# Kernel tuning notes

Measured on AMD Instinct MI355X. Metric: run time of the kernel, lower is better.

## Reference

```python
import jax, jax.numpy as jnp
import numpy as np

HEADS = 16
HEAD_DIM = 64
HIDDEN = HEADS * HEAD_DIM          # 1024
EXP = 4
QKVFF = HIDDEN * (3 + EXP)         # 7168
VFF = HIDDEN * (1 + EXP)           # 5120
B, L = 2, 2048
LN_EPS = 1e-5


def setup_inputs() -> dict:
    key = jax.random.key(0)
    k1, k2, k3 = jax.random.split(key, 3)
    x = jax.random.normal(k1, (B, L, HIDDEN), dtype=jnp.float32)
    W_in = jax.random.normal(k2, (HIDDEN, QKVFF), dtype=jnp.float32) * (HIDDEN ** -0.5)
    W_out = jax.random.normal(k3, (VFF, HIDDEN), dtype=jnp.float32) * (VFF ** -0.5)
    ln_w = jnp.ones((HIDDEN,), dtype=jnp.float32)
    ln_b = jnp.zeros((HIDDEN,), dtype=jnp.float32)
    return {"x": x, "ln_w": ln_w, "ln_b": ln_b, "W_in": W_in, "W_out": W_out}


def _rotary_tables(l, dtype):
    inv_freq = 1.0 / (10000.0 ** (jnp.arange(0, HEAD_DIM, 2, dtype=jnp.float32) / HEAD_DIM))
    t = jnp.arange(l, dtype=jnp.float32)
    freqs = t[:, None] * inv_freq[None, :]            # [l, d/2]
    emb = jnp.concatenate([freqs, freqs], axis=-1)     # [l, d]
    return jnp.cos(emb).astype(dtype), jnp.sin(emb).astype(dtype)


def _rotate_half(x):
    x1, x2 = jnp.split(x, 2, axis=-1)
    return jnp.concatenate([-x2, x1], axis=-1)


def reference(x, ln_w, ln_b, W_in, W_out):
    b, l, d = x.shape
    # shared LayerNorm
    mu = jnp.mean(x, axis=-1, keepdims=True)
    var = jnp.var(x, axis=-1, keepdims=True)
    xn = (x - mu) * jax.lax.rsqrt(var + LN_EPS) * ln_w + ln_b
    # fused in-projection
    h = xn @ W_in                                      # [b, l, qkvff]
    q, k, v, ff = jnp.split(h, [HIDDEN, 2 * HIDDEN, 3 * HIDDEN], axis=-1)
    q = q.reshape(b, l, HEADS, HEAD_DIM)
    k = k.reshape(b, l, HEADS, HEAD_DIM)
    v = v.reshape(b, l, HEADS, HEAD_DIM)
    # inline RoPE on q, k
    cos, sin = _rotary_tables(l, x.dtype)              # [l, d]
    cos = cos[None, :, None, :]
    sin = sin[None, :, None, :]
    q = q * cos + _rotate_half(q) * sin
    k = k * cos + _rotate_half(k) * sin
    # causal attention with explicit mask bias (as in the original)
    a = jnp.einsum('bihd,bjhd->bhij', q, k) * (HEAD_DIM ** -0.5)
    causal = jnp.tril(jnp.ones((l, l), dtype=a.dtype))
    a = a + (-1e10) * (1.0 - causal)
    a = jax.nn.softmax(a, axis=-1)
    o = jnp.einsum('bhij,bjhd->bihd', a, v).reshape(b, l, HIDDEN)
    # parallel FF branch
    ff = jax.nn.gelu(ff, approximate=False)
    return jnp.concatenate([o, ff], axis=-1) @ W_out
```

## Files before the change

### kernel.cpp

```cpp
#include <hip/hip_runtime.h>
#include <math.h>

#define HEADS 16
#define HEAD_DIM 64
#define HIDDEN 1024
#define NQKVFF 7168
#define VFF 5120
#define SEQ 2048
#define MROWS 4096

typedef unsigned short u16;
typedef __attribute__((ext_vector_type(8))) short bf16x8;
typedef __attribute__((ext_vector_type(4))) float f32x4;
typedef __attribute__((address_space(1))) void gas_void;
typedef __attribute__((address_space(3))) void las_void;

__device__ inline u16 f2bf(float f) {
    union { float f; unsigned u; } v; v.f = f;
    unsigned r = v.u + 0x7FFFu + ((v.u >> 16) & 1u);
    return (u16)(r >> 16);
}
__device__ inline float bf2f(u16 h) {
    union { unsigned u; float f; } v; v.u = ((unsigned)h) << 16;
    return v.f;
}

__global__ __launch_bounds__(256) void ln_kernel(const float* __restrict__ x,
        const float* __restrict__ w, const float* __restrict__ b,
        u16* __restrict__ xn) {
    int row = blockIdx.x;
    int tid = threadIdx.x;
    const float* xr = x + (size_t)row * HIDDEN;
    float4 v = ((const float4*)xr)[tid];
    float s = v.x + v.y + v.z + v.w;
    float sq = v.x * v.x + v.y * v.y + v.z * v.z + v.w * v.w;
    for (int off = 32; off > 0; off >>= 1) {
        s += __shfl_down(s, off, 64);
        sq += __shfl_down(sq, off, 64);
    }
    __shared__ float ls[4], lsq[4];
    int wid = tid >> 6, lane = tid & 63;
    if (lane == 0) { ls[wid] = s; lsq[wid] = sq; }
    __syncthreads();
    float ts = ls[0] + ls[1] + ls[2] + ls[3];
    float tsq = lsq[0] + lsq[1] + lsq[2] + lsq[3];
    float mu = ts * (1.0f / HIDDEN);
    float var = tsq * (1.0f / HIDDEN) - mu * mu;
    float rstd = rsqrtf(var + 1e-5f);
    float4 wv = ((const float4*)w)[tid];
    float4 bv = ((const float4*)b)[tid];
    ushort4 o;
    o.x = f2bf((v.x - mu) * rstd * wv.x + bv.x);
    o.y = f2bf((v.y - mu) * rstd * wv.y + bv.y);
    o.z = f2bf((v.z - mu) * rstd * wv.z + bv.z);
    o.w = f2bf((v.w - mu) * rstd * wv.w + bv.w);
    ((ushort4*)(xn + (size_t)row * HIDDEN))[tid] = o;
}

__global__ __launch_bounds__(256) void transpose_f2b(const float* __restrict__ in,
        u16* __restrict__ out, int R, int C) {
    __shared__ u16 tile[32][33];
    int c0 = blockIdx.x * 32, r0 = blockIdx.y * 32;
    int tx = threadIdx.x & 31, ty = threadIdx.x >> 5;
#pragma unroll
    for (int k = 0; k < 4; k++)
        tile[ty + k * 8][tx] = f2bf(in[(size_t)(r0 + ty + k * 8) * C + c0 + tx]);
    __syncthreads();
#pragma unroll
    for (int k = 0; k < 4; k++)
        out[(size_t)(c0 + ty + k * 8) * R + r0 + tx] = tile[tx][ty + k * 8];
}

__global__ __launch_bounds__(256) void transpose_v(const u16* __restrict__ h3,
        u16* __restrict__ out) {
    __shared__ u16 tile[32][33];
    int bh = blockIdx.x, it = blockIdx.y, dt = blockIdx.z;
    int bb = bh >> 4, hh = bh & 15;
    u16* dst = out + (size_t)bh * HEAD_DIM * SEQ;
    int tx = threadIdx.x & 31, ty = threadIdx.x >> 5;
    int i0 = it * 32, d0 = dt * 32;
#pragma unroll
    for (int k = 0; k < 4; k++)
        tile[ty + k * 8][tx] = h3[(size_t)(bb * 2048 + i0 + ty + k * 8) * 3072 + 2048 + hh * 64 + d0 + tx];
    __syncthreads();
#pragma unroll
    for (int k = 0; k < 4; k++) {
        int d = d0 + ty + k * 8;
        int i = i0 + tx;
        dst[(size_t)(i >> 5) * 2048 + (d >> 4) * 512 +
            ((((i & 31) >> 3) * 16) + (d & 15)) * 8 + (i & 7)] = tile[tx][ty + k * 8];
    }
}

__global__ __launch_bounds__(256) void rope_kernel(const u16* __restrict__ h3,
        u16* __restrict__ qk) {
    int idx = blockIdx.x * 256 + threadIdx.x;
    int j = idx & 31;
    int i = (idx >> 5) & 2047;
    int rest = idx >> 16;
    int t = rest >> 5, bh = rest & 31;
    int bb = bh >> 4, hh = bh & 15;
    const u16* src = h3 + ((size_t)(bb * 2048 + i)) * 3072 + t * 1024 + hh * 64;
    float x1 = bf2f(src[j]), x2 = bf2f(src[j + 32]);
    float f = expf(j * -0.28782313662425572f);
    float ang = i * f;
    float s, c;
    sincosf(ang, &s, &c);
    float scale = (t == 0) ? 0.18033688011112043f : 1.0f;
    u16* base = qk + (size_t)rest * (SEQ * HEAD_DIM);
    int off = (i >> 4) * 1024 + ((j >> 3) * 16 + (i & 15)) * 8 + (j & 7);
    base[off]       = f2bf((x1 * c - x2 * s) * scale);
    base[off + 512] = f2bf((x2 * c + x1 * s) * scale);
}

__device__ inline void gemm_core_128(const u16* __restrict__ A, int lda,
                                     const u16* __restrict__ BT, int ldb,
                                     int Klen, int bm, int bn, f32x4 acc[4][4],
                                     u16* ldsA, u16* ldsB) {
    const int tid = threadIdx.x;
    const int wid = tid >> 6;
    const int lane = tid & 63;
    const int quad = lane >> 4;
    const int cc = lane & 15;
    const int wm = (wid >> 1) * 64;
    const int wn = (wid & 1) * 64;
#pragma unroll
    for (int i = 0; i < 4; i++)
#pragma unroll
        for (int j = 0; j < 4; j++)
#pragma unroll
            for (int r = 0; r < 4; r++) acc[i][j][r] = 0.0f;

    const int row = tid >> 2;
    const int gch = ((tid & 3) ^ ((row >> 1) & 3)) * 8;
    const int slot = (quad ^ ((cc >> 1) & 3)) * 8;
    for (int k0 = 0; k0 < Klen; k0 += 32) {
        __syncthreads();
#pragma unroll
        for (int I = 0; I < 2; I++) {
            int r128 = I * 64 + row;
            const u16* ga = A + (size_t)(bm + r128) * lda + k0 + gch;
            u16* la = ldsA + ((size_t)(I * 256 + (tid & 192))) * 8;
            __builtin_amdgcn_global_load_lds((gas_void*)ga, (las_void*)la, 16, 0, 0);
            const u16* gb = BT + (size_t)(bn + r128) * ldb + k0 + gch;
            u16* lb = ldsB + ((size_t)(I * 256 + (tid & 192))) * 8;
            __builtin_amdgcn_global_load_lds((gas_void*)gb, (las_void*)lb, 16, 0, 0);
        }
        __syncthreads();
        bf16x8 af[4], bfr[4];
#pragma unroll
        for (int t = 0; t < 4; t++) {
            af[t]  = *(const bf16x8*)(ldsA + (wm + t * 16 + cc) * 32 + slot);
            bfr[t] = *(const bf16x8*)(ldsB + (wn + t * 16 + cc) * 32 + slot);
        }
#pragma unroll
        for (int i = 0; i < 4; i++)
#pragma unroll
            for (int j = 0; j < 4; j++)
                acc[i][j] = __builtin_amdgcn_mfma_f32_16x16x32_bf16(af[i], bfr[j], acc[i][j], 0, 0, 0);
    }
}

__device__ inline float gelu_f(float v) {
    float u = v * (v * v * 0.044715f + 1.0f) * 0.7978845608028654f;
    u = fminf(u, 15.0f);
    float e = exp2f(u * 2.8853900817779268f);
    return v * (e / (e + 1.0f));
}

__global__ __launch_bounds__(256) void gemm1(const u16* __restrict__ xn,
        const u16* __restrict__ WinT, u16* __restrict__ h3, u16* __restrict__ a2) {
    __shared__ u16 ldsA[128 * 32];
    __shared__ u16 ldsB[128 * 32];
    int bm = blockIdx.x * 128, bn = blockIdx.y * 128;
    f32x4 acc[4][4];
    gemm_core_128(xn, HIDDEN, WinT, HIDDEN, HIDDEN, bm, bn, acc, ldsA, ldsB);
    const int tid = threadIdx.x, wid = tid >> 6, lane = tid & 63;
    const int quad = lane >> 4, cc = lane & 15;
    const int wm = (wid >> 1) * 64, wn = (wid & 1) * 64;
    const bool isff = (bn >= 3072);
#pragma unroll
    for (int i = 0; i < 4; i++)
#pragma unroll
        for (int j = 0; j < 4; j++)
#pragma unroll
            for (int r = 0; r < 4; r++) {
                int m = bm + wm + i * 16 + quad * 4 + r;
                int n = bn + wn + j * 16 + cc;
                float v = acc[i][j][r];
                if (isff) {
                    a2[(size_t)m * VFF + (n - 2048)] = f2bf(gelu_f(v));
                } else {
                    h3[(size_t)m * 3072 + n] = f2bf(v);
                }
            }
}

__global__ __launch_bounds__(256) void gemm2(const u16* __restrict__ a2,
        const u16* __restrict__ WoutT, float* __restrict__ p0, float* __restrict__ p1) {
    __shared__ u16 ldsA[128 * 32];
    __shared__ u16 ldsB[128 * 32];
    int bm = blockIdx.x * 128, bn = blockIdx.y * 128;
    int split = blockIdx.z;
    float* dst = split ? p1 : p0;
    f32x4 acc[4][4];
    gemm_core_128(a2 + split * 2560, VFF, WoutT + split * 2560, VFF, 2560,
                  bm, bn, acc, ldsA, ldsB);
    const int tid = threadIdx.x, wid = tid >> 6, lane = tid & 63;
    const int quad = lane >> 4, cc = lane & 15;
    const int wm = (wid >> 1) * 64, wn = (wid & 1) * 64;
#pragma unroll
    for (int i = 0; i < 4; i++)
#pragma unroll
        for (int j = 0; j < 4; j++)
#pragma unroll
            for (int r = 0; r < 4; r++) {
                int m = bm + wm + i * 16 + quad * 4 + r;
                int n = bn + wn + j * 16 + cc;
                dst[(size_t)m * HIDDEN + n] = acc[i][j][r];
            }
}

__global__ __launch_bounds__(256) void reduce2(const float* __restrict__ p0,
        const float* __restrict__ p1, float* __restrict__ out) {
    int i = blockIdx.x * 256 + threadIdx.x;
    float4 a = ((const float4*)p0)[i];
    float4 b = ((const float4*)p1)[i];
    a.x += b.x; a.y += b.y; a.z += b.z; a.w += b.w;
    ((float4*)out)[i] = a;
}

__global__ __launch_bounds__(256) void attn_kernel(const u16* __restrict__ qk,
        const u16* __restrict__ vt, u16* __restrict__ a2) {
    const int id  = blockIdx.x;
    const int bh  = (id & 7) * 4 + ((id >> 3) & 3);
    const int bx  = id >> 5;
    const int tid = threadIdx.x;
    const int wid = tid >> 6;
    const int lane = tid & 63;
    const int quad = lane >> 4;
    const int cc = lane & 15;
    const int slot = wid >> 1;
    const int parity = wid & 1;
    const int tile = slot ? (127 - bx) : bx;
    const int q0 = tile * 16;

    const u16* Qp = qk + (size_t)bh * (SEQ * HEAD_DIM);
    const u16* Kp = qk + (size_t)(32 + bh) * (SEQ * HEAD_DIM);
    const u16* VP = vt + (size_t)bh * (HEAD_DIM * SEQ);

    __shared__ u16 Pbuf[4][16 * 72];
    __shared__ float obuf[2][64 * 17];
    __shared__ float lbuf[2][16];
    u16* P = Pbuf[wid];

    const int bb = bh >> 4, hh = bh & 15;
    const int qcol = q0 + cc;

    bf16x8 qa0 = *(const bf16x8*)(Qp + (q0 >> 4) * 1024 + lane * 8);
    bf16x8 qa1 = *(const bf16x8*)(Qp + (q0 >> 4) * 1024 + 512 + lane * 8);

    float ps = 0.0f;
    f32x4 ot[4];
#pragma unroll
    for (int mt = 0; mt < 4; mt++)
#pragma unroll
        for (int r = 0; r < 4; r++) ot[mt][r] = 0.0f;

    for (int kb = parity * 64; kb < q0 + 16; kb += 128) {
        const bool diag = (kb + 64 > q0);
        f32x4 s[4];
        __builtin_amdgcn_s_setprio(1);
#pragma unroll
        for (int c = 0; c < 4; c++) {
            s[c][0] = -32.0f; s[c][1] = -32.0f; s[c][2] = -32.0f; s[c][3] = -32.0f;
            const u16* kblob = Kp + ((kb >> 4) + c) * 1024 + lane * 8;
            bf16x8 ka0 = *(const bf16x8*)(kblob);
            bf16x8 ka1 = *(const bf16x8*)(kblob + 512);
            s[c] = __builtin_amdgcn_mfma_f32_16x16x32_bf16(ka0, qa0, s[c], 0, 0, 0);
            s[c] = __builtin_amdgcn_mfma_f32_16x16x32_bf16(ka1, qa1, s[c], 0, 0, 0);
        }
        __builtin_amdgcn_s_setprio(0);
        bf16x8 vf[2][4];
#pragma unroll
        for (int kc = 0; kc < 2; kc++)
#pragma unroll
            for (int mt = 0; mt < 4; mt++)
                vf[kc][mt] = *(const bf16x8*)(VP + ((kb >> 5) + kc) * 2048 + mt * 512 + lane * 8);
        if (diag) {
#pragma unroll
            for (int c = 0; c < 4; c++)
#pragma unroll
                for (int r = 0; r < 4; r++) {
                    int key = kb + c * 16 + quad * 4 + r;
                    s[c][r] = (key <= qcol) ? s[c][r] : -10000.0f;
                }
        }
#pragma unroll
        for (int c = 0; c < 4; c++) {
            float p0v = exp2f(s[c][0]); ps += p0v;
            float p1v = exp2f(s[c][1]); ps += p1v;
            float p2v = exp2f(s[c][2]); ps += p2v;
            float p3v = exp2f(s[c][3]); ps += p3v;
            unsigned r0, r1;
            asm("v_cvt_pk_bf16_f32 %0, %1, %2" : "=v"(r0) : "v"(p0v), "v"(p1v));
            asm("v_cvt_pk_bf16_f32 %0, %1, %2" : "=v"(r1) : "v"(p2v), "v"(p3v));
            uint2 pk; pk.x = r0; pk.y = r1;
            *(uint2*)(P + cc * 72 + c * 16 + quad * 4) = pk;
        }
        asm volatile("s_waitcnt lgkmcnt(0)" ::: "memory");
        __builtin_amdgcn_s_setprio(1);
#pragma unroll
        for (int kc = 0; kc < 2; kc++) {
            bf16x8 pb = *(const bf16x8*)(P + cc * 72 + kc * 32 + quad * 8);
#pragma unroll
            for (int mt = 0; mt < 4; mt++)
                ot[mt] = __builtin_amdgcn_mfma_f32_16x16x32_bf16(vf[kc][mt], pb, ot[mt], 0, 0, 0);
        }
        __builtin_amdgcn_s_setprio(0);
    }

    ps += __shfl_xor(ps, 16, 64);
    ps += __shfl_xor(ps, 32, 64);

    if (parity == 1) {
        if (quad == 0) lbuf[slot][cc] = ps;
        float* ob = obuf[slot] + lane * 17;
#pragma unroll
        for (int mt = 0; mt < 4; mt++)
#pragma unroll
            for (int r = 0; r < 4; r++) ob[mt * 4 + r] = ot[mt][r];
    }
    __syncthreads();
    if (parity == 0) {
        float l = ps + lbuf[slot][cc];
        float rl = 1.0f / l;
        const float* ob = obuf[slot] + lane * 17;
        u16* dst = a2 + ((size_t)(bb * SEQ + q0 + cc)) * VFF + hh * 64;
#pragma unroll
        for (int mt = 0; mt < 4; mt++) {
            ushort4 o;
            o.x = f2bf((ot[mt][0] + ob[mt * 4 + 0]) * rl);
            o.y = f2bf((ot[mt][1] + ob[mt * 4 + 1]) * rl);
            o.z = f2bf((ot[mt][2] + ob[mt * 4 + 2]) * rl);
            o.w = f2bf((ot[mt][3] + ob[mt * 4 + 3]) * rl);
            *(ushort4*)(dst + mt * 16 + quad * 4) = o;
        }
    }
}

extern "C" void kernel_launch(void* const* d_in, const int* in_sizes, int n_in,
                              void* d_out, int out_size, void* d_ws, size_t ws_size,
                              hipStream_t stream) {
    const float* x     = (const float*)d_in[0];
    const float* ln_w  = (const float*)d_in[1];
    const float* ln_b  = (const float*)d_in[2];
    const float* W_in  = (const float*)d_in[3];
    const float* W_out = (const float*)d_in[4];
    float* out = (float*)d_out;
    char* ws = (char*)d_ws;
    u16* xn    = (u16*)(ws);
    u16* WinT  = (u16*)(ws + 8388608);
    u16* h3    = (u16*)(ws + 25165824);
    u16* WoutT = (u16*)(ws + 50331648);
    u16* a2    = (u16*)(ws + 60817408);
    u16* qkb   = (u16*)(ws);
    u16* vtb   = (u16*)(ws + 16777216);
    float* p0  = (float*)(ws + 25165824);
    float* p1  = (float*)(ws);

    ln_kernel<<<dim3(MROWS), dim3(256), 0, stream>>>(x, ln_w, ln_b, xn);
    transpose_f2b<<<dim3(NQKVFF / 32, HIDDEN / 32), dim3(256), 0, stream>>>(W_in, WinT, HIDDEN, NQKVFF);
    transpose_f2b<<<dim3(HIDDEN / 32, VFF / 32), dim3(256), 0, stream>>>(W_out, WoutT, VFF, HIDDEN);
    gemm1<<<dim3(MROWS / 128, NQKVFF / 128), dim3(256), 0, stream>>>(xn, WinT, h3, a2);
    rope_kernel<<<dim3(16384), dim3(256), 0, stream>>>(h3, qkb);
    transpose_v<<<dim3(32, SEQ / 32, HEAD_DIM / 32), dim3(256), 0, stream>>>(h3, vtb);
    attn_kernel<<<dim3(2048), dim3(256), 0, stream>>>(qkb, vtb, a2);
    gemm2<<<dim3(MROWS / 128, HIDDEN / 128, 2), dim3(256), 0, stream>>>(a2, WoutT, p0, p1);
    reduce2<<<dim3(MROWS * HIDDEN / 4 / 256), dim3(256), 0, stream>>>(p0, p1, out);
}
```

Baseline: 326.3 us.

## Fuse RoPE and V transpose into gemm1 epilogue, drop h3 buffer

The RoPE rotation for q/k and the V transpose into the attention-friendly tiled layout now happen directly in the gemm1 epilogue. This removes the rope_kernel and transpose_v launches and the round trip through the intermediate h3 buffer. The workspace is re-laid out to match. The cost is heavier epilogue work with sincos and scattered stores inside the GEMM, and fast __sincosf replaces sincosf, which may lose accuracy at large angles.

```diff
diff --git a/kernel.cpp b/kernel.cpp
--- a/kernel.cpp
+++ b/kernel.cpp
@@ -71,48 +71,6 @@
         out[(size_t)(c0 + ty + k * 8) * R + r0 + tx] = tile[tx][ty + k * 8];
 }
 
-__global__ __launch_bounds__(256) void transpose_v(const u16* __restrict__ h3,
-        u16* __restrict__ out) {
-    __shared__ u16 tile[32][33];
-    int bh = blockIdx.x, it = blockIdx.y, dt = blockIdx.z;
-    int bb = bh >> 4, hh = bh & 15;
-    u16* dst = out + (size_t)bh * HEAD_DIM * SEQ;
-    int tx = threadIdx.x & 31, ty = threadIdx.x >> 5;
-    int i0 = it * 32, d0 = dt * 32;
-#pragma unroll
-    for (int k = 0; k < 4; k++)
-        tile[ty + k * 8][tx] = h3[(size_t)(bb * 2048 + i0 + ty + k * 8) * 3072 + 2048 + hh * 64 + d0 + tx];
-    __syncthreads();
-#pragma unroll
-    for (int k = 0; k < 4; k++) {
-        int d = d0 + ty + k * 8;
-        int i = i0 + tx;
-        dst[(size_t)(i >> 5) * 2048 + (d >> 4) * 512 +
-            ((((i & 31) >> 3) * 16) + (d & 15)) * 8 + (i & 7)] = tile[tx][ty + k * 8];
-    }
-}
-
-__global__ __launch_bounds__(256) void rope_kernel(const u16* __restrict__ h3,
-        u16* __restrict__ qk) {
-    int idx = blockIdx.x * 256 + threadIdx.x;
-    int j = idx & 31;
-    int i = (idx >> 5) & 2047;
-    int rest = idx >> 16;
-    int t = rest >> 5, bh = rest & 31;
-    int bb = bh >> 4, hh = bh & 15;
-    const u16* src = h3 + ((size_t)(bb * 2048 + i)) * 3072 + t * 1024 + hh * 64;
-    float x1 = bf2f(src[j]), x2 = bf2f(src[j + 32]);
-    float f = expf(j * -0.28782313662425572f);
-    float ang = i * f;
-    float s, c;
-    sincosf(ang, &s, &c);
-    float scale = (t == 0) ? 0.18033688011112043f : 1.0f;
-    u16* base = qk + (size_t)rest * (SEQ * HEAD_DIM);
-    int off = (i >> 4) * 1024 + ((j >> 3) * 16 + (i & 15)) * 8 + (j & 7);
-    base[off]       = f2bf((x1 * c - x2 * s) * scale);
-    base[off + 512] = f2bf((x2 * c + x1 * s) * scale);
-}
-
 __device__ inline void gemm_core_128(const u16* __restrict__ A, int lda,
                                      const u16* __restrict__ BT, int ldb,
                                      int Klen, int bm, int bn, f32x4 acc[4][4],
@@ -169,7 +127,8 @@
 }
 
 __global__ __launch_bounds__(256) void gemm1(const u16* __restrict__ xn,
-        const u16* __restrict__ WinT, u16* __restrict__ h3, u16* __restrict__ a2) {
+        const u16* __restrict__ WinT, u16* __restrict__ qkb,
+        u16* __restrict__ vtb, u16* __restrict__ a2) {
     __shared__ u16 ldsA[128 * 32];
     __shared__ u16 ldsB[128 * 32];
     int bm = blockIdx.x * 128, bn = blockIdx.y * 128;
@@ -178,22 +137,64 @@
     const int tid = threadIdx.x, wid = tid >> 6, lane = tid & 63;
     const int quad = lane >> 4, cc = lane & 15;
     const int wm = (wid >> 1) * 64, wn = (wid & 1) * 64;
-    const bool isff = (bn >= 3072);
-#pragma unroll
-    for (int i = 0; i < 4; i++)
-#pragma unroll
-        for (int j = 0; j < 4; j++)
+    const int m0 = bm + wm;
+    const int b = m0 >> 11;
+
+    if (bn >= 3072) {
+#pragma unroll
+        for (int i = 0; i < 4; i++)
+#pragma unroll
+            for (int j = 0; j < 4; j++)
+#pragma unroll
+                for (int r = 0; r < 4; r++) {
+                    int m = m0 + i * 16 + quad * 4 + r;
+                    int n = bn + wn + j * 16 + cc;
+                    a2[(size_t)m * VFF + (n - 2048)] = f2bf(gelu_f(acc[i][j][r]));
+                }
+    } else if (bn >= 2048) {
+        int hh = ((bn - 2048 + wn) >> 6) & 15;
+        u16* dst = vtb + (size_t)(b * 16 + hh) * (HEAD_DIM * SEQ);
+#pragma unroll
+        for (int i = 0; i < 4; i++) {
+            int key0 = (m0 + i * 16 + quad * 4) & 2047;
+            size_t ob = (size_t)(key0 >> 5) * 2048 +
+                        (((key0 & 31) >> 3) * 16 + cc) * 8 + (key0 & 7);
+#pragma unroll
+            for (int jf = 0; jf < 4; jf++) {
+                ushort4 o;
+                o.x = f2bf(acc[i][jf][0]);
+                o.y = f2bf(acc[i][jf][1]);
+                o.z = f2bf(acc[i][jf][2]);
+                o.w = f2bf(acc[i][jf][3]);
+                *(ushort4*)(dst + ob + jf * 512) = o;
+            }
+        }
+    } else {
+        int t = bn >> 10;
+        int hh = ((bn + wn) >> 6) & 15;
+        u16* base = qkb + (size_t)(t * 32 + b * 16 + hh) * (SEQ * HEAD_DIM);
+        float scale = t ? 1.0f : 0.18033688011112043f;
+        float f0 = expf(cc * -0.28782313662425572f);
+        float f1 = expf((16 + cc) * -0.28782313662425572f);
+        const int o0 = ((cc >> 3) * 16) * 8 + (cc & 7);
+        const int o1 = ((2 + (cc >> 3)) * 16) * 8 + (cc & 7);
+#pragma unroll
+        for (int i = 0; i < 4; i++)
 #pragma unroll
             for (int r = 0; r < 4; r++) {
-                int m = bm + wm + i * 16 + quad * 4 + r;
-                int n = bn + wn + j * 16 + cc;
-                float v = acc[i][j][r];
-                if (isff) {
-                    a2[(size_t)m * VFF + (n - 2048)] = f2bf(gelu_f(v));
-                } else {
-                    h3[(size_t)m * 3072 + n] = f2bf(v);
-                }
+                int pos = (m0 + i * 16 + quad * 4 + r) & 2047;
+                int ob = (pos >> 4) * 1024 + (pos & 15) * 8;
+                float s_, c_;
+                __sincosf(pos * f0, &s_, &c_);
+                float x1 = acc[i][0][r], x2 = acc[i][2][r];
+                base[ob + o0]       = f2bf((x1 * c_ - x2 * s_) * scale);
+                base[ob + o0 + 512] = f2bf((x2 * c_ + x1 * s_) * scale);
+                __sincosf(pos * f1, &s_, &c_);
+                x1 = acc[i][1][r]; x2 = acc[i][3][r];
+                base[ob + o1]       = f2bf((x1 * c_ - x2 * s_) * scale);
+                base[ob + o1 + 512] = f2bf((x2 * c_ + x1 * s_) * scale);
             }
+    }
 }
 
 __global__ __launch_bounds__(256) void gemm2(const u16* __restrict__ a2,
@@ -361,20 +362,17 @@
     char* ws = (char*)d_ws;
     u16* xn    = (u16*)(ws);
     u16* WinT  = (u16*)(ws + 8388608);
-    u16* h3    = (u16*)(ws + 25165824);
-    u16* WoutT = (u16*)(ws + 50331648);
-    u16* a2    = (u16*)(ws + 60817408);
-    u16* qkb   = (u16*)(ws);
-    u16* vtb   = (u16*)(ws + 16777216);
-    float* p0  = (float*)(ws + 25165824);
-    float* p1  = (float*)(ws);
+    u16* qkb   = (u16*)(ws + 23068672);
+    u16* vtb   = (u16*)(ws + 39845888);
+    u16* WoutT = (u16*)(ws + 48234496);
+    u16* a2    = (u16*)(ws + 58720256);
+    float* p0  = (float*)(ws);
+    float* p1  = (float*)(ws + 16777216);
 
     ln_kernel<<<dim3(MROWS), dim3(256), 0, stream>>>(x, ln_w, ln_b, xn);
     transpose_f2b<<<dim3(NQKVFF / 32, HIDDEN / 32), dim3(256), 0, stream>>>(W_in, WinT, HIDDEN, NQKVFF);
     transpose_f2b<<<dim3(HIDDEN / 32, VFF / 32), dim3(256), 0, stream>>>(W_out, WoutT, VFF, HIDDEN);
-    gemm1<<<dim3(MROWS / 128, NQKVFF / 128), dim3(256), 0, stream>>>(xn, WinT, h3, a2);
-    rope_kernel<<<dim3(16384), dim3(256), 0, stream>>>(h3, qkb);
-    transpose_v<<<dim3(32, SEQ / 32, HEAD_DIM / 32), dim3(256), 0, stream>>>(h3, vtb);
+    gemm1<<<dim3(MROWS / 128, NQKVFF / 128), dim3(256), 0, stream>>>(xn, WinT, qkb, vtb, a2);
     attn_kernel<<<dim3(2048), dim3(256), 0, stream>>>(qkb, vtb, a2);
     gemm2<<<dim3(MROWS / 128, HIDDEN / 128, 2), dim3(256), 0, stream>>>(a2, WoutT, p0, p1);
     reduce2<<<dim3(MROWS * HIDDEN / 4 / 256), dim3(256), 0, stream>>>(p0, p1, out);
```

Result: faster. 318.3 us (-2.5%).
